# Performance work log

Hardware: AMD Instinct MI355X
Metric: run time of the kernel (lower is better)

The kernel has to match this reference:

```python
import jax, jax.numpy as jnp
import numpy as np

TEMPERATURE = 0.07
NI = 4  # num_instance


def setup_inputs() -> dict:
    key = jax.random.key(0)
    features = jax.random.normal(key, (4096, 2048, 4), dtype=jnp.float32)
    return {"features": features}


def reference(features):
    b, c, t = features.shape
    # (t==8 path not exercised: t=4 here, matching the module's post-reshape shape)
    ni = NI
    g = b // ni
    n = t * ni
    # (g, ni, c, t) -> (g, t, ni, c) -> (g, t*ni, c)
    f = features.reshape(g, ni, c, t).transpose(0, 3, 1, 2).reshape(g, n, c)
    # F.normalize(dim=-1) with eps clamp
    norm = jnp.linalg.norm(f, axis=-1, keepdims=True)
    f = f / jnp.maximum(norm, 1e-12)

    labels = jnp.repeat(jnp.arange(t), ni)  # (n,)
    mask = (labels[:, None] == labels[None, :]).astype(f.dtype)  # (n, n)
    mask_pos = mask * (1.0 - jnp.eye(n, dtype=f.dtype))  # positives, excl. self

    cos = jnp.einsum('gic,gjc->gij', f, f)  # (g, n, n) cosine similarity
    logits = cos / TEMPERATURE
    exp_logits = jnp.exp(logits)
    exp_neg = jnp.sum(exp_logits * (1.0 - mask)[None], axis=-1, keepdims=True)
    log_prob = logits - jnp.log(exp_neg + exp_logits)
    # torch mask_pos.sum() is over the single (n, n) matrix (broadcast over groups)
    loss = -jnp.sum(log_prob * mask_pos[None]) / jnp.sum(mask_pos)
    return loss
```

## Files before the change

### kernel.cpp

```cpp
#include <hip/hip_runtime.h>
#include <math.h>


#define NGROUP 1024
#define C 2048
#define NPAIR 136

__device__ __forceinline__ constexpr int pair_idx(int i, int j) {
    return i * 16 - (i * (i - 1)) / 2 + (j - i);
}

__global__ __launch_bounds__(128, 2)
void infonce_group_kernel(const float4* __restrict__ feats,
                          float* __restrict__ gloss) {
    const int g    = blockIdx.x;
    const int tid  = threadIdx.x;
    const int lane = tid & 63;
    const int wid  = tid >> 6;

    float acc[NPAIR];
#pragma unroll
    for (int p = 0; p < NPAIR; ++p) acc[p] = 0.f;

    const float4* base = feats + (size_t)g * 4 * C;

    for (int it = 0; it < C / 128; ++it) {
        const int c = tid + it * 128;
        const float4 v0 = base[0 * C + c];
        const float4 v1 = base[1 * C + c];
        const float4 v2 = base[2 * C + c];
        const float4 v3 = base[3 * C + c];
        const float r[16] = { v0.x, v1.x, v2.x, v3.x,
                              v0.y, v1.y, v2.y, v3.y,
                              v0.z, v1.z, v2.z, v3.z,
                              v0.w, v1.w, v2.w, v3.w };
#pragma unroll
        for (int i = 0; i < 16; ++i)
#pragma unroll
            for (int j = i; j < 16; ++j)
                acc[pair_idx(i, j)] = fmaf(r[i], r[j], acc[pair_idx(i, j)]);
    }

#pragma unroll
    for (int p = 0; p < NPAIR; ++p) {
        float v = acc[p];
        v += __shfl_xor(v, 1);
        v += __shfl_xor(v, 2);
        v += __shfl_xor(v, 4);
        v += __shfl_xor(v, 8);
        v += __shfl_xor(v, 16);
        v += __shfl_xor(v, 32);
        acc[p] = v;
    }

    __shared__ float wsum[2][NPAIR];
    __shared__ float S[16][17];
    __shared__ float rowloss[16];

#pragma unroll
    for (int p = 0; p < NPAIR; ++p) {
        if (lane == (p & 63)) wsum[wid][p] = acc[p];
    }
    __syncthreads();

    for (int p = tid; p < NPAIR; p += 128) {
        int i = 0, rem = p;
        while (rem >= 16 - i) { rem -= 16 - i; ++i; }
        const int j = i + rem;
        const float s = wsum[0][p] + wsum[1][p];
        S[i][j] = s;
        S[j][i] = s;
    }
    __syncthreads();

    if (tid < 16) {
        const int i = tid;
        const float inv_i = 1.0f / fmaxf(sqrtf(S[i][i]), 1e-12f);
        float logits_row[16];
        float expneg = 0.f;
#pragma unroll
        for (int j = 0; j < 16; ++j) {
            const float inv_j = 1.0f / fmaxf(sqrtf(S[j][j]), 1e-12f);
            const float cosv = S[i][j] * inv_i * inv_j;
            const float lg = cosv / 0.07f;
            logits_row[j] = lg;
            if ((j >> 2) != (i >> 2)) expneg += expf(lg);
        }
        float sum = 0.f;
#pragma unroll
        for (int j = 0; j < 16; ++j) {
            if ((j >> 2) == (i >> 2) && j != i) {
                const float lg = logits_row[j];
                sum += lg - logf(expneg + expf(lg));
            }
        }
        rowloss[i] = sum;
    }
    __syncthreads();

    if (tid == 0) {
        float t = 0.f;
#pragma unroll
        for (int i = 0; i < 16; ++i) t += rowloss[i];
        gloss[g] = t;
    }
}

__global__ void infonce_final_reduce(const float* __restrict__ gloss,
                                     float* __restrict__ out) {
    const int tid = threadIdx.x;
    float s = 0.f;
    for (int i = tid; i < NGROUP; i += 256) s += gloss[i];
    s += __shfl_xor(s, 1);
    s += __shfl_xor(s, 2);
    s += __shfl_xor(s, 4);
    s += __shfl_xor(s, 8);
    s += __shfl_xor(s, 16);
    s += __shfl_xor(s, 32);
    __shared__ float ws[4];
    const int lane = tid & 63, wid = tid >> 6;
    if (lane == 0) ws[wid] = s;
    __syncthreads();
    if (tid == 0) {
        const float t = ws[0] + ws[1] + ws[2] + ws[3];
        out[0] = -t / 48.0f;
    }
}

extern "C" void kernel_launch(void* const* d_in, const int* in_sizes, int n_in,
                              void* d_out, int out_size, void* d_ws, size_t ws_size,
                              hipStream_t stream) {
    const float4* feats = (const float4*)d_in[0];
    float* gloss = (float*)d_ws;
    float* out = (float*)d_out;

    infonce_group_kernel<<<NGROUP, 128, 0, stream>>>(feats, gloss);
    infonce_final_reduce<<<1, 256, 0, stream>>>(gloss, out);
}
```

Baseline: 56.91 us.

## Split channel reduction across four blocks per group with separate finish kernel

Each group's 2048-channel Gram accumulation is split into four blocks, giving 4096 blocks instead of 1024 so more blocks run in parallel across the GPU. Each block preloads all four of its iterations' float4 loads up front to expose memory-level parallelism. The 136 partial pair sums per block go to workspace, and a new finish kernel adds the four partials and computes the per-group loss. This adds an extra kernel launch, a workspace round trip, and more register pressure from the preloaded values.

```diff
diff --git a/kernel.cpp b/kernel.cpp
--- a/kernel.cpp
+++ b/kernel.cpp
@@ -5,35 +5,43 @@
 #define NGROUP 1024
 #define C 2048
 #define NPAIR 136
+#define SPLIT 4
+#define CPB (C / SPLIT)
+#define ITER (CPB / 128)
 
 __device__ __forceinline__ constexpr int pair_idx(int i, int j) {
     return i * 16 - (i * (i - 1)) / 2 + (j - i);
 }
 
 __global__ __launch_bounds__(128, 2)
-void infonce_group_kernel(const float4* __restrict__ feats,
-                          float* __restrict__ gloss) {
-    const int g    = blockIdx.x;
+void infonce_partial_kernel(const float4* __restrict__ feats,
+                            float* __restrict__ psum) {
+    const int blk  = blockIdx.x;
+    const int g    = blk >> 2;
+    const int s    = blk & 3;
     const int tid  = threadIdx.x;
     const int lane = tid & 63;
     const int wid  = tid >> 6;
+
+    const float4* base = feats + (size_t)g * 4 * C + s * CPB + tid;
+
+    float4 v[ITER][4];
+#pragma unroll
+    for (int it = 0; it < ITER; ++it)
+#pragma unroll
+        for (int row = 0; row < 4; ++row)
+            v[it][row] = base[row * C + it * 128];
 
     float acc[NPAIR];
 #pragma unroll
     for (int p = 0; p < NPAIR; ++p) acc[p] = 0.f;
 
-    const float4* base = feats + (size_t)g * 4 * C;
-
-    for (int it = 0; it < C / 128; ++it) {
-        const int c = tid + it * 128;
-        const float4 v0 = base[0 * C + c];
-        const float4 v1 = base[1 * C + c];
-        const float4 v2 = base[2 * C + c];
-        const float4 v3 = base[3 * C + c];
-        const float r[16] = { v0.x, v1.x, v2.x, v3.x,
-                              v0.y, v1.y, v2.y, v3.y,
-                              v0.z, v1.z, v2.z, v3.z,
-                              v0.w, v1.w, v2.w, v3.w };
+#pragma unroll
+    for (int it = 0; it < ITER; ++it) {
+        const float r[16] = { v[it][0].x, v[it][1].x, v[it][2].x, v[it][3].x,
+                              v[it][0].y, v[it][1].y, v[it][2].y, v[it][3].y,
+                              v[it][0].z, v[it][1].z, v[it][2].z, v[it][3].z,
+                              v[it][0].w, v[it][1].w, v[it][2].w, v[it][3].w };
 #pragma unroll
         for (int i = 0; i < 16; ++i)
 #pragma unroll
@@ -43,31 +51,47 @@
 
 #pragma unroll
     for (int p = 0; p < NPAIR; ++p) {
-        float v = acc[p];
-        v += __shfl_xor(v, 1);
-        v += __shfl_xor(v, 2);
-        v += __shfl_xor(v, 4);
-        v += __shfl_xor(v, 8);
-        v += __shfl_xor(v, 16);
-        v += __shfl_xor(v, 32);
-        acc[p] = v;
+        float x = acc[p];
+        x += __shfl_xor(x, 1);
+        x += __shfl_xor(x, 2);
+        x += __shfl_xor(x, 4);
+        x += __shfl_xor(x, 8);
+        x += __shfl_xor(x, 16);
+        x += __shfl_xor(x, 32);
+        acc[p] = x;
     }
 
     __shared__ float wsum[2][NPAIR];
-    __shared__ float S[16][17];
-    __shared__ float rowloss[16];
-
 #pragma unroll
     for (int p = 0; p < NPAIR; ++p) {
         if (lane == (p & 63)) wsum[wid][p] = acc[p];
     }
     __syncthreads();
 
+    float* dst = psum + (size_t)blk * NPAIR;
+    for (int p = tid; p < NPAIR; p += 128)
+        dst[p] = wsum[0][p] + wsum[1][p];
+}
+
+__global__ __launch_bounds__(128)
+void infonce_group_finish(const float* __restrict__ psum,
+                          float* __restrict__ gloss) {
+    const int g   = blockIdx.x;
+    const int tid = threadIdx.x;
+
+    __shared__ float S[16][17];
+    __shared__ float rowloss[16];
+
+    const float* p0 = psum + (size_t)(g * 4 + 0) * NPAIR;
+    const float* p1 = psum + (size_t)(g * 4 + 1) * NPAIR;
+    const float* p2 = psum + (size_t)(g * 4 + 2) * NPAIR;
+    const float* p3 = psum + (size_t)(g * 4 + 3) * NPAIR;
+
     for (int p = tid; p < NPAIR; p += 128) {
         int i = 0, rem = p;
         while (rem >= 16 - i) { rem -= 16 - i; ++i; }
         const int j = i + rem;
-        const float s = wsum[0][p] + wsum[1][p];
+        const float s = p0[p] + p1[p] + p2[p] + p3[p];
         S[i][j] = s;
         S[j][i] = s;
     }
@@ -131,9 +155,11 @@
                               void* d_out, int out_size, void* d_ws, size_t ws_size,
                               hipStream_t stream) {
     const float4* feats = (const float4*)d_in[0];
-    float* gloss = (float*)d_ws;
-    float* out = (float*)d_out;
+    float* psum  = (float*)d_ws;
+    float* gloss = psum + (size_t)NGROUP * SPLIT * NPAIR;
+    float* out   = (float*)d_out;
 
-    infonce_group_kernel<<<NGROUP, 128, 0, stream>>>(feats, gloss);
+    infonce_partial_kernel<<<NGROUP * SPLIT, 128, 0, stream>>>(feats, psum);
+    infonce_group_finish<<<NGROUP, 128, 0, stream>>>(psum, gloss);
     infonce_final_reduce<<<1, 256, 0, stream>>>(gloss, out);
 }
```

Result: slower. 168.7 us (+196.5%).
